# Performance work log

Measured on AMD Instinct MI355X. Metric: run time of the kernel, lower is better.

The kernel has to match this reference:

```python
import jax, jax.numpy as jnp
import numpy as np

B, S, D, H, E, K = 4, 2048, 1024, 4096, 8, 2
CAP = 2048      # expert capacity (tokens)
ALPHA = 0.01    # load-balance loss coefficient


def setup_inputs() -> dict:
    key = jax.random.key(0)
    ks = jax.random.split(key, 8)
    def w(k, shape, fan_in):
        return jax.random.normal(k, shape, jnp.float32) * (fan_in ** -0.5)
    return {
        "input": jax.random.normal(ks[0], (B, S, D), jnp.float32),
        "rw": w(ks[1], (D, E), D), "rb": jnp.zeros((E,), jnp.float32),
        "w1": w(ks[2], (E, D, H), D), "b1": jnp.zeros((E, H), jnp.float32),
        "w2": w(ks[3], (E, H, D), H), "b2": jnp.zeros((E, D), jnp.float32),
        "ow1": w(ks[4], (D, H), D), "ob1": jnp.zeros((H,), jnp.float32),
        "ow2": w(ks[5], (H, D), H), "ob2": jnp.zeros((D,), jnp.float32),
    }


def _moe(x, rw, rb, w1, b1, w2, b2, ow1, ob1, ow2, ob2):
    Bx, Sx, Dx = x.shape
    N = Bx * Sx
    xf = x.reshape(N, Dx)

    # --- router: softmax -> top-k -> renormalize ---
    scores = jax.nn.softmax(xf @ rw + rb, axis=-1)          # [N,E]
    tw, ti = jax.lax.top_k(scores, K)                       # [N,K]
    tw = tw / tw.sum(-1, keepdims=True)
    onehot = jax.nn.one_hot(ti, E, dtype=xf.dtype)          # [N,K,E]
    w_ne = jnp.einsum('nk,nke->ne', tw, onehot)             # combine weight per (token, expert)
    mask = onehot.sum(1) > 0                                # [N,E]
    mi = mask.astype(jnp.int32)

    # exclusive rank of each token within its expert's queue (token order, as torch nonzero())
    rank = jnp.cumsum(mi, axis=0) - mi                      # [N,E]
    within = mask & (rank < CAP)
    over = mask & (rank >= CAP)

    # --- dispatch within-capacity tokens into [E, CAP] slots (sentinel = N) ---
    tok = jnp.broadcast_to(jnp.arange(N, dtype=jnp.int32)[:, None], (N, E))
    eid = jnp.broadcast_to(jnp.arange(E, dtype=jnp.int32)[None, :], (N, E))
    slot = jnp.where(within, rank, CAP)                     # non-assigned -> pad column
    buf = jnp.full((E, CAP + 1), N, dtype=jnp.int32)
    buf = buf.at[eid.reshape(-1), slot.reshape(-1)].set(tok.reshape(-1))
    buf = buf[:, :CAP]                                      # [E,CAP]

    xpad = jnp.concatenate([xf, jnp.zeros((1, Dx), xf.dtype)], axis=0)
    xd = xpad[buf]                                          # [E,CAP,D]

    # --- grouped expert FFN (Linear -> relu -> Linear) ---
    h = jax.nn.relu(jnp.einsum('ecd,edh->ech', xd, w1) + b1[:, None, :])
    y = jnp.einsum('ech,ehd->ecd', h, w2) + b2[:, None, :]  # [E,CAP,D]

    # combine weights gathered per slot; pad slots get weight 0
    wpad = jnp.concatenate([w_ne, jnp.zeros((1, E), w_ne.dtype)], axis=0)
    wc = wpad[buf, jnp.arange(E, dtype=jnp.int32)[:, None]]  # [E,CAP]

    outpad = jnp.zeros((N + 1, Dx), xf.dtype)
    outpad = outpad.at[buf.reshape(-1)].add((wc[..., None] * y).reshape(-1, Dx))
    out = outpad[:N]

    # --- overflow tokens -> shared overflow FFN (computed densely, masked by weight) ---
    w_of = (w_ne * over.astype(w_ne.dtype)).sum(-1)          # [N]
    yo = jax.nn.relu(xf @ ow1 + ob1) @ ow2 + ob2             # [N,D]
    out = out + w_of[:, None] * yo

    # --- aux load-balance loss (detached in torch via .item()) ---
    num = mi.sum(0)                                          # [E]
    cnt = jnp.minimum(num, CAP)
    f = cnt.astype(xf.dtype) / N
    p = (w_ne * within.astype(w_ne.dtype)).sum(0) / jnp.maximum(cnt, 1).astype(xf.dtype)
    aux = ALPHA * E * jnp.sum(f * p)
    return out.reshape(Bx, Sx, Dx), jax.lax.stop_gradient(aux)


def reference(input, rw, rb, w1, b1, w2, b2, ow1, ob1, ow2, ob2):
    return _moe(input, rw, rb, w1, b1, w2, b2, ow1, ob1, ow2, ob2)
```

## Files before the change

### kernel.cpp

```cpp
#include <hip/hip_runtime.h>
#include <cstdint>

typedef __attribute__((ext_vector_type(8))) short bf16x8;
typedef __attribute__((ext_vector_type(4))) float f32x4;

#define N_TOK    8192
#define DMODEL   1024
#define HDIM     4096
#define CAPACITY 2048

__device__ __forceinline__ unsigned short f2bf(float f) {
  unsigned u = __float_as_uint(f);
  u += 0x7FFFu + ((u >> 16) & 1u);
  return (unsigned short)(u >> 16);
}

__device__ __forceinline__ void gl_lds16(const unsigned short* g, unsigned short* l) {
  __builtin_amdgcn_global_load_lds(
      (const __attribute__((address_space(1))) void*)g,
      (__attribute__((address_space(3))) void*)l, 16, 0, 0);
}

__global__ void cvtx_kernel(const float* __restrict__ x, unsigned short* __restrict__ xb) {
  long i0 = ((long)blockIdx.x * 256 + threadIdx.x) * 16;
#pragma unroll
  for (int ii = 0; ii < 4; ii++) {
    float4 v = *(const float4*)(x + i0 + ii * 4);
    ushort4 u;
    u.x = f2bf(v.x); u.y = f2bf(v.y); u.z = f2bf(v.z); u.w = f2bf(v.w);
    *(ushort4*)(xb + i0 + ii * 4) = u;
  }
}

__global__ void router_kernel(const float* __restrict__ x, const float* __restrict__ rw,
                              const float* __restrict__ rb, int4* __restrict__ recs) {
  int wave = threadIdx.x >> 6;
  int lane = threadIdx.x & 63;
  int tok = blockIdx.x * 4 + wave;
  const float* xr = x + (long)tok * DMODEL;
  float s[8];
#pragma unroll
  for (int e = 0; e < 8; e++) s[e] = 0.f;
  for (int ii = 0; ii < DMODEL / 64; ii++) {
    int k = lane + 64 * ii;
    float xv = xr[k];
    const float* wr = rw + k * 8;
    float4 a = *(const float4*)wr;
    float4 b = *(const float4*)(wr + 4);
    s[0] += xv * a.x; s[1] += xv * a.y; s[2] += xv * a.z; s[3] += xv * a.w;
    s[4] += xv * b.x; s[5] += xv * b.y; s[6] += xv * b.z; s[7] += xv * b.w;
  }
#pragma unroll
  for (int m = 1; m < 64; m <<= 1) {
#pragma unroll
    for (int e = 0; e < 8; e++) s[e] += __shfl_xor(s[e], m);
  }
  if (lane == 0) {
#pragma unroll
    for (int e = 0; e < 8; e++) s[e] += rb[e];
    int b0 = 0; float v0 = s[0];
#pragma unroll
    for (int e = 1; e < 8; e++) if (s[e] > v0) { v0 = s[e]; b0 = e; }
    int b1 = -1; float v1 = 0.f;
#pragma unroll
    for (int e = 0; e < 8; e++) {
      if (e == b0) continue;
      if (b1 < 0 || s[e] > v1) { v1 = s[e]; b1 = e; }
    }
    float t0 = 1.f / (1.f + expf(v1 - v0));
    float t1 = 1.f - t0;
    recs[tok] = make_int4(b0, b1, __float_as_int(t0), __float_as_int(t1));
  }
}

__device__ __forceinline__ int bump16(uint4& v, int e) {
  unsigned sh = (e & 1) ? 16u : 0u;
  unsigned inc = 1u << sh;
  unsigned old;
  switch (e >> 1) {
    case 0: old = v.x; v.x += inc; break;
    case 1: old = v.y; v.y += inc; break;
    case 2: old = v.z; v.z += inc; break;
    default: old = v.w; v.w += inc; break;
  }
  return (int)((old >> sh) & 0xFFFFu);
}

__device__ __forceinline__ unsigned field16(uint4 v, int e) {
  unsigned w;
  switch (e >> 1) { case 0: w = v.x; break; case 1: w = v.y; break; case 2: w = v.z; break; default: w = v.w; break; }
  return (w >> ((e & 1) ? 16 : 0)) & 0xFFFFu;
}

__global__ void assign_kernel(const int4* __restrict__ recs, int* __restrict__ buf,
                              float* __restrict__ wc, int* __restrict__ cnt,
                              float* __restrict__ auxOut) {
  __shared__ uint4 sc[1024];
  __shared__ unsigned sco[1024];
  __shared__ float pnum[8];
  int tid = threadIdx.x;
  if (tid < 8) pnum[tid] = 0.f;
  int4 rc[8];
#pragma unroll
  for (int i = 0; i < 8; i++) {
    rc[i] = recs[tid * 8 + i];
    rc[i].x &= 7; rc[i].y &= 7;
  }
  uint4 c; c.x = c.y = c.z = c.w = 0u;
#pragma unroll
  for (int i = 0; i < 8; i++) { bump16(c, rc[i].x); bump16(c, rc[i].y); }
  sc[tid] = c;
  __syncthreads();
  for (int off = 1; off < 1024; off <<= 1) {
    uint4 v; v.x = v.y = v.z = v.w = 0u;
    if (tid >= off) v = sc[tid - off];
    __syncthreads();
    sc[tid].x += v.x; sc[tid].y += v.y; sc[tid].z += v.z; sc[tid].w += v.w;
    __syncthreads();
  }
  uint4 base; base.x = base.y = base.z = base.w = 0u;
  if (tid > 0) base = sc[tid - 1];
  uint4 totals = sc[1023];

  uint4 run = base;
  float wof[8];
  unsigned oc = 0;
#pragma unroll
  for (int i = 0; i < 8; i++) {
    int tk = tid * 8 + i;
    int e0 = rc[i].x, e1 = rc[i].y;
    float w0 = __int_as_float(rc[i].z);
    float w1 = __int_as_float(rc[i].w);
    float w = 0.f;
    int r0 = bump16(run, e0);
    if (r0 < CAPACITY) {
      buf[e0 * CAPACITY + r0] = tk;
      wc[e0 * CAPACITY + r0] = w0;
      atomicAdd(&pnum[e0], w0);
    } else w += w0;
    int r1 = bump16(run, e1);
    if (r1 < CAPACITY) {
      buf[e1 * CAPACITY + r1] = tk;
      wc[e1 * CAPACITY + r1] = w1;
      atomicAdd(&pnum[e1], w1);
    } else w += w1;
    wof[i] = w;
    if (w > 0.f) oc++;
  }
  sco[tid] = oc;
  __syncthreads();
  for (int off = 1; off < 1024; off <<= 1) {
    unsigned v = (tid >= off) ? sco[tid - off] : 0u;
    __syncthreads();
    sco[tid] += v;
    __syncthreads();
  }
  unsigned ob = (tid > 0) ? sco[tid - 1] : 0u;
  unsigned Ot = sco[1023];
#pragma unroll
  for (int i = 0; i < 8; i++) {
    if (wof[i] > 0.f) {
      unsigned slot = ob++;
      int ve = 8 + (int)(slot >> 11);
      buf[ve * CAPACITY + (int)(slot & 2047)] = tid * 8 + i;
      wc[ve * CAPACITY + (int)(slot & 2047)] = wof[i];
    }
  }
  __syncthreads();
  if (tid == 0) {
    float aux = 0.f;
#pragma unroll
    for (int e = 0; e < 8; e++) {
      int tot = (int)field16(totals, e);
      int c2 = tot < CAPACITY ? tot : CAPACITY;
      cnt[e] = c2;
      float f = (float)c2 / (float)N_TOK;
      float p = pnum[e] / (float)(c2 > 1 ? c2 : 1);
      aux += f * p;
    }
#pragma unroll
    for (int i = 0; i < 4; i++) {
      int c2 = (int)Ot - i * CAPACITY;
      c2 = c2 < 0 ? 0 : (c2 > CAPACITY ? CAPACITY : c2);
      cnt[8 + i] = c2;
    }
    auxOut[0] = 0.01f * 8.f * aux;
  }
}

__global__ __launch_bounds__(256) void transpose_all(
    const float* __restrict__ w1, const float* __restrict__ w2,
    const float* __restrict__ ow1, const float* __restrict__ ow2,
    unsigned short* __restrict__ wt1, unsigned short* __restrict__ wt2,
    long slotStride, int pairBase) {
  int pair = pairBase + blockIdx.x / 2048;
  int t = blockIdx.x & 2047;
  long srcOff = (long)pair * DMODEL * HDIM;
  long dstOff = (long)(blockIdx.x / 2048) * slotStride;
  const float* in; unsigned short* out; int R, C;
  if (t < 1024) {
    in = (pair < 8) ? w1 + srcOff : ow1;
    out = wt1 + dstOff;
    R = DMODEL; C = HDIM;
  } else {
    in = (pair < 8) ? w2 + srcOff : ow2;
    out = wt2 + dstOff;
    R = HDIM; C = DMODEL;
    t -= 1024;
  }
  int tr = t / (C >> 6);
  int tc = t % (C >> 6);
  int r0 = tr << 6, c0 = tc << 6;
  __shared__ float tl[64][65];
  int row = threadIdx.x >> 4, cg = threadIdx.x & 15;
#pragma unroll
  for (int i = 0; i < 4; i++) {
    int r = row + 16 * i;
    float4 v = *(const float4*)(in + (long)(r0 + r) * C + c0 + cg * 4);
    tl[r][cg * 4 + 0] = v.x; tl[r][cg * 4 + 1] = v.y;
    tl[r][cg * 4 + 2] = v.z; tl[r][cg * 4 + 3] = v.w;
  }
  __syncthreads();
#pragma unroll
  for (int i = 0; i < 4; i++) {
    int oc = row + 16 * i;
    ushort4 o;
    o.x = f2bf(tl[cg * 4 + 0][oc]);
    o.y = f2bf(tl[cg * 4 + 1][oc]);
    o.z = f2bf(tl[cg * 4 + 2][oc]);
    o.w = f2bf(tl[cg * 4 + 3][oc]);
    *(ushort4*)(out + (long)(c0 + oc) * R + r0 + cg * 4) = o;
  }
}

__global__ __launch_bounds__(256) void gemm1_kernel(
    const unsigned short* __restrict__ xb, const int* __restrict__ buf,
    const int* __restrict__ cnt, const unsigned short* __restrict__ wt1, long wtStride,
    const float* __restrict__ b1, const float* __restrict__ ob1,
    unsigned short* __restrict__ h, long hStride, int eBase,
    const unsigned short* __restrict__ zp) {
  int q = gridDim.x >> 3;
  int bx = blockIdx.x;
  int id = (bx & 7) * q + (bx >> 3);
  int e = eBase + (id >> 9);
  int rem = id & 511;
  int mb = rem >> 5, nb = rem & 31;
  int m0 = mb * 128, n0 = nb * 128;
  if (m0 >= cnt[e]) return;
  const int* bufe = buf + e * CAPACITY;
  int slot = e < 8 ? e : 8;
  const unsigned short* wte = wt1 + (long)slot * wtStride;
  const float* bias = (e < 8) ? b1 + (long)e * HDIM : ob1;
  unsigned short* he = h + (long)e * hStride;

  __shared__ unsigned short As[128 * 64];
  __shared__ unsigned short Bs[128 * 64];

  int tid = threadIdx.x;
  int wave = tid >> 6, lane = tid & 63;
  int l15 = lane & 15, hi = lane >> 4;
  int mo = (wave >> 1) * 64, no = (wave & 1) * 64;

  int rlo = lane >> 3;
  int cg = (lane & 7) ^ rlo;
  const unsigned short* asrc[4];
  const unsigned short* bsrc[4];
#pragma unroll
  for (int j = 0; j < 4; j++) {
    int r = wave * 32 + j * 8 + rlo;
    int tok = bufe[m0 + r];
    asrc[j] = ((unsigned)tok < (unsigned)N_TOK) ? (xb + (long)tok * DMODEL + cg * 8)
                                                : (zp + cg * 8);
    bsrc[j] = wte + (long)(n0 + r) * DMODEL + cg * 8;
  }

  f32x4 zero4 = {0.f, 0.f, 0.f, 0.f};
  f32x4 acc[4][4];
#pragma unroll
  for (int mi = 0; mi < 4; mi++)
#pragma unroll
    for (int ni = 0; ni < 4; ni++) acc[mi][ni] = zero4;

  for (int k0 = 0; k0 < DMODEL; k0 += 64) {
#pragma unroll
    for (int j = 0; j < 4; j++) {
      gl_lds16(asrc[j] + k0, &As[wave * 2048 + j * 512]);
      gl_lds16(bsrc[j] + k0, &Bs[wave * 2048 + j * 512]);
    }
    __syncthreads();
#pragma unroll
    for (int ks = 0; ks < 2; ks++) {
      bf16x8 af[4], bfr[4];
#pragma unroll
      for (int mi = 0; mi < 4; mi++) {
        int r = mo + mi * 16 + l15;
        af[mi] = *(bf16x8*)&As[r * 64 + (((ks * 4 + hi) ^ (r & 7)) << 3)];
      }
#pragma unroll
      for (int ni = 0; ni < 4; ni++) {
        int r = no + ni * 16 + l15;
        bfr[ni] = *(bf16x8*)&Bs[r * 64 + (((ks * 4 + hi) ^ (r & 7)) << 3)];
      }
#pragma unroll
      for (int mi = 0; mi < 4; mi++)
#pragma unroll
        for (int ni = 0; ni < 4; ni++)
          acc[mi][ni] = __builtin_amdgcn_mfma_f32_16x16x32_bf16(af[mi], bfr[ni], acc[mi][ni], 0, 0, 0);
    }
    __syncthreads();
  }
#pragma unroll
  for (int ni = 0; ni < 4; ni++) {
    int col = n0 + no + ni * 16 + l15;
    float bv = bias[col];
#pragma unroll
    for (int mi = 0; mi < 4; mi++) {
#pragma unroll
      for (int j = 0; j < 4; j++) {
        int mr = m0 + mo + mi * 16 + hi * 4 + j;
        float val = acc[mi][ni][j] + bv;
        val = val > 0.f ? val : 0.f;
        he[(long)mr * HDIM + col] = f2bf(val);
      }
    }
  }
}

__global__ __launch_bounds__(256) void gemm2_kernel(
    const unsigned short* __restrict__ h, long hStride,
    const unsigned short* __restrict__ wt2, long wtStride,
    const float* __restrict__ b2, const float* __restrict__ ob2,
    const int* __restrict__ buf, const float* __restrict__ wc,
    const int* __restrict__ cnt, float* __restrict__ out,
    int eBase, int per, int klen) {
  int q = gridDim.x >> 3;
  int bx = blockIdx.x;
  int id = (bx & 7) * q + (bx >> 3);
  int e = eBase + id / per;
  int rem = id % per;
  int tile = rem & 127;
  int kc = rem >> 7;
  int mb = tile >> 3, nb = tile & 7;
  int m0 = mb * 128, n0 = nb * 128;
  if (m0 >= cnt[e]) return;
  const int* bufe = buf + e * CAPACITY;
  const float* wce = wc + e * CAPACITY;
  int slot = e < 8 ? e : 8;
  const unsigned short* wte = wt2 + (long)slot * wtStride;
  const float* bias = (e < 8) ? b2 + (long)e * DMODEL : ob2;
  const unsigned short* he = h + (long)e * hStride;
  int kbase = kc * klen;

  __shared__ unsigned short As[128 * 64];
  __shared__ unsigned short Bs[128 * 64];

  int tid = threadIdx.x;
  int wave = tid >> 6, lane = tid & 63;
  int l15 = lane & 15, hi = lane >> 4;
  int mo = (wave >> 1) * 64, no = (wave & 1) * 64;

  int rlo = lane >> 3;
  int cg = (lane & 7) ^ rlo;
  const unsigned short* asrc[4];
  const unsigned short* bsrc[4];
#pragma unroll
  for (int j = 0; j < 4; j++) {
    int r = wave * 32 + j * 8 + rlo;
    asrc[j] = he + (long)(m0 + r) * HDIM + cg * 8;
    bsrc[j] = wte + (long)(n0 + r) * HDIM + cg * 8;
  }

  f32x4 zero4 = {0.f, 0.f, 0.f, 0.f};
  f32x4 acc[4][4];
#pragma unroll
  for (int mi = 0; mi < 4; mi++)
#pragma unroll
    for (int ni = 0; ni < 4; ni++) acc[mi][ni] = zero4;

  for (int k0 = kbase; k0 < kbase + klen; k0 += 64) {
#pragma unroll
    for (int j = 0; j < 4; j++) {
      gl_lds16(asrc[j] + k0, &As[wave * 2048 + j * 512]);
      gl_lds16(bsrc[j] + k0, &Bs[wave * 2048 + j * 512]);
    }
    __syncthreads();
#pragma unroll
    for (int ks = 0; ks < 2; ks++) {
      bf16x8 af[4], bfr[4];
#pragma unroll
      for (int mi = 0; mi < 4; mi++) {
        int r = mo + mi * 16 + l15;
        af[mi] = *(bf16x8*)&As[r * 64 + (((ks * 4 + hi) ^ (r & 7)) << 3)];
      }
#pragma unroll
      for (int ni = 0; ni < 4; ni++) {
        int r = no + ni * 16 + l15;
        bfr[ni] = *(bf16x8*)&Bs[r * 64 + (((ks * 4 + hi) ^ (r & 7)) << 3)];
      }
#pragma unroll
      for (int mi = 0; mi < 4; mi++)
#pragma unroll
        for (int ni = 0; ni < 4; ni++)
          acc[mi][ni] = __builtin_amdgcn_mfma_f32_16x16x32_bf16(af[mi], bfr[ni], acc[mi][ni], 0, 0, 0);
    }
    __syncthreads();
  }
  float bcol[4];
#pragma unroll
  for (int ni = 0; ni < 4; ni++)
    bcol[ni] = (kc == 0) ? bias[n0 + no + ni * 16 + l15] : 0.f;
#pragma unroll
  for (int mi = 0; mi < 4; mi++) {
#pragma unroll
    for (int j = 0; j < 4; j++) {
      int m = m0 + mo + mi * 16 + hi * 4 + j;
      int t = bufe[m];
      if ((unsigned)t >= (unsigned)N_TOK) continue;
      float wv = wce[m];
      float* orow = out + (long)t * DMODEL;
#pragma unroll
      for (int ni = 0; ni < 4; ni++) {
        int col = n0 + no + ni * 16 + l15;
        float val = wv * (acc[mi][ni][j] + bcol[ni]);
        atomicAdd(orow + col, val);
      }
    }
  }
}

extern "C" void kernel_launch(void* const* d_in, const int* in_sizes, int n_in,
                              void* d_out, int out_size, void* d_ws, size_t ws_size,
                              hipStream_t stream) {
  const float* x   = (const float*)d_in[0];
  const float* rw  = (const float*)d_in[1];
  const float* rb  = (const float*)d_in[2];
  const float* w1  = (const float*)d_in[3];
  const float* b1  = (const float*)d_in[4];
  const float* w2  = (const float*)d_in[5];
  const float* b2  = (const float*)d_in[6];
  const float* ow1 = (const float*)d_in[7];
  const float* ob1 = (const float*)d_in[8];
  const float* ow2 = (const float*)d_in[9];
  const float* ob2 = (const float*)d_in[10];
  float* out = (float*)d_out;

  const long WSLOT = (long)DMODEL * HDIM;
  const long HSLOT = (long)CAPACITY * HDIM;

  bool fused = ws_size >= 380ull * 1024 * 1024;

  char* ws = (char*)d_ws;
  int4* recs = (int4*)(ws);
  int*  buf  = (int*)(ws + 131072);
  float* wcp = (float*)(ws + 229376);
  int*  cnt  = (int*)(ws + 327680);
  unsigned short* zp = (unsigned short*)(ws + 331776);
  unsigned short* xb  = (unsigned short*)(ws + 1048576);
  unsigned short* wt1 = (unsigned short*)(ws + 17825792);
  unsigned short* wt2;
  unsigned short* h;
  if (fused) {
    wt2 = (unsigned short*)(ws + 93323264);
    h   = (unsigned short*)(ws + 168820736);
  } else {
    wt2 = (unsigned short*)(ws + 26214400);
    h   = (unsigned short*)(ws + 34603008);
  }

  hipMemsetAsync(d_out, 0, (size_t)out_size * sizeof(float), stream);
  hipMemsetAsync(buf, 0xFF, 12 * CAPACITY * sizeof(int), stream);
  hipMemsetAsync(wcp, 0, 12 * CAPACITY * sizeof(float), stream);
  hipMemsetAsync(zp, 0, 2048, stream);

  cvtx_kernel<<<2048, 256, 0, stream>>>(x, xb);
  router_kernel<<<2048, 256, 0, stream>>>(x, rw, rb, recs);
  assign_kernel<<<1, 1024, 0, stream>>>(recs, buf, wcp, cnt, out + (long)N_TOK * DMODEL);

  if (fused) {
    transpose_all<<<9 * 2048, 256, 0, stream>>>(w1, w2, ow1, ow2, wt1, wt2, WSLOT, 0);
    gemm1_kernel<<<12 * 512, 256, 0, stream>>>(xb, buf, cnt, wt1, WSLOT, b1, ob1, h, HSLOT, 0, zp);
    gemm2_kernel<<<12 * 128, 256, 0, stream>>>(h, HSLOT, wt2, WSLOT, b2, ob2, buf, wcp, cnt, out,
                                               0, 128, HDIM);
  } else {
    for (int e = 0; e < 12; e++) {
      if (e <= 8)
        transpose_all<<<2048, 256, 0, stream>>>(w1, w2, ow1, ow2, wt1, wt2, 0, e);
      gemm1_kernel<<<512, 256, 0, stream>>>(xb, buf, cnt, wt1, 0, b1, ob1, h, 0, e, zp);
      gemm2_kernel<<<512, 256, 0, stream>>>(h, 0, wt2, 0, b2, ob2, buf, wcp, cnt, out,
                                            e, 512, HDIM / 4);
    }
  }
}
```

Baseline: 685.2 us.

## Use 256x256 tiles with 512-thread blocks and double-buffered LDS in expert GEMMs

Both expert GEMM kernels move from 128x128 tiles with 4 waves to 256x256 tiles with 8 waves, each wave owning a 128x64 sub-tile. The LDS staging is now double-buffered so the next K-slice loads while MFMAs run on the current one. The aim is more operand reuse per global byte and overlapping of loads with compute. GEMM2 split-K drops from 4 to 2 chunks, and the launch grids shrink to match. The costs are 128 KB of LDS per block and a much larger register footprint (128 accumulator floats plus fragments). Under launch_bounds(512,2) that footprint risks register spills and limits occupancy to one block per CU.

```diff
diff --git a/kernel.cpp b/kernel.cpp
--- a/kernel.cpp
+++ b/kernel.cpp
@@ -233,7 +233,16 @@
   }
 }
 
-__global__ __launch_bounds__(256) void gemm1_kernel(
+
+#define STAGE_PAIR(Abuf, Bbuf, kk)                                  \
+  do {                                                              \
+    _Pragma("unroll") for (int s = 0; s < 4; s++) {                 \
+      gl_lds16(asrc[s] + (kk), &(Abuf)[wave * 2048 + s * 512]);     \
+      gl_lds16(bsrc[s] + (kk), &(Bbuf)[wave * 2048 + s * 512]);     \
+    }                                                               \
+  } while (0)
+
+__global__ __launch_bounds__(512, 2) void gemm1_kernel(
     const unsigned short* __restrict__ xb, const int* __restrict__ buf,
     const int* __restrict__ cnt, const unsigned short* __restrict__ wt1, long wtStride,
     const float* __restrict__ b1, const float* __restrict__ ob1,
@@ -242,10 +251,10 @@
   int q = gridDim.x >> 3;
   int bx = blockIdx.x;
   int id = (bx & 7) * q + (bx >> 3);
-  int e = eBase + (id >> 9);
-  int rem = id & 511;
-  int mb = rem >> 5, nb = rem & 31;
-  int m0 = mb * 128, n0 = nb * 128;
+  int e = eBase + id / 128;
+  int rem = id % 128;
+  int mb = rem >> 4, nb = rem & 15;
+  int m0 = mb * 256, n0 = nb * 256;
   if (m0 >= cnt[e]) return;
   const int* bufe = buf + e * CAPACITY;
   int slot = e < 8 ? e : 8;
@@ -253,68 +262,74 @@
   const float* bias = (e < 8) ? b1 + (long)e * HDIM : ob1;
   unsigned short* he = h + (long)e * hStride;
 
-  __shared__ unsigned short As[128 * 64];
-  __shared__ unsigned short Bs[128 * 64];
+  __shared__ unsigned short As[2][256 * 64];
+  __shared__ unsigned short Bs[2][256 * 64];
 
   int tid = threadIdx.x;
   int wave = tid >> 6, lane = tid & 63;
   int l15 = lane & 15, hi = lane >> 4;
-  int mo = (wave >> 1) * 64, no = (wave & 1) * 64;
+  int wr = wave >> 2, wc = wave & 3;
+  int mo = wr * 128, no = wc * 64;
 
   int rlo = lane >> 3;
   int cg = (lane & 7) ^ rlo;
   const unsigned short* asrc[4];
   const unsigned short* bsrc[4];
 #pragma unroll
-  for (int j = 0; j < 4; j++) {
-    int r = wave * 32 + j * 8 + rlo;
+  for (int s = 0; s < 4; s++) {
+    int r = wave * 32 + s * 8 + rlo;
     int tok = bufe[m0 + r];
-    asrc[j] = ((unsigned)tok < (unsigned)N_TOK) ? (xb + (long)tok * DMODEL + cg * 8)
+    asrc[s] = ((unsigned)tok < (unsigned)N_TOK) ? (xb + (long)tok * DMODEL + cg * 8)
                                                 : (zp + cg * 8);
-    bsrc[j] = wte + (long)(n0 + r) * DMODEL + cg * 8;
+    bsrc[s] = wte + (long)(n0 + r) * DMODEL + cg * 8;
   }
 
   f32x4 zero4 = {0.f, 0.f, 0.f, 0.f};
-  f32x4 acc[4][4];
-#pragma unroll
-  for (int mi = 0; mi < 4; mi++)
+  f32x4 acc[8][4];
+#pragma unroll
+  for (int mi = 0; mi < 8; mi++)
 #pragma unroll
     for (int ni = 0; ni < 4; ni++) acc[mi][ni] = zero4;
 
-  for (int k0 = 0; k0 < DMODEL; k0 += 64) {
-#pragma unroll
-    for (int j = 0; j < 4; j++) {
-      gl_lds16(asrc[j] + k0, &As[wave * 2048 + j * 512]);
-      gl_lds16(bsrc[j] + k0, &Bs[wave * 2048 + j * 512]);
-    }
-    __syncthreads();
+  const int NT = DMODEL / 64;
+  STAGE_PAIR(As[0], Bs[0], 0);
+  __syncthreads();
+  int cur = 0;
+  for (int t = 0; t < NT; t++) {
+    if (t + 1 < NT) {
+      if (cur) STAGE_PAIR(As[0], Bs[0], (t + 1) * 64);
+      else     STAGE_PAIR(As[1], Bs[1], (t + 1) * 64);
+    }
+    const unsigned short* Ac = As[cur];
+    const unsigned short* Bc = Bs[cur];
 #pragma unroll
     for (int ks = 0; ks < 2; ks++) {
-      bf16x8 af[4], bfr[4];
-#pragma unroll
-      for (int mi = 0; mi < 4; mi++) {
+      bf16x8 af[8], bfv[4];
+#pragma unroll
+      for (int mi = 0; mi < 8; mi++) {
         int r = mo + mi * 16 + l15;
-        af[mi] = *(bf16x8*)&As[r * 64 + (((ks * 4 + hi) ^ (r & 7)) << 3)];
+        af[mi] = *(bf16x8*)&Ac[r * 64 + (((ks * 4 + hi) ^ (r & 7)) << 3)];
       }
 #pragma unroll
       for (int ni = 0; ni < 4; ni++) {
         int r = no + ni * 16 + l15;
-        bfr[ni] = *(bf16x8*)&Bs[r * 64 + (((ks * 4 + hi) ^ (r & 7)) << 3)];
+        bfv[ni] = *(bf16x8*)&Bc[r * 64 + (((ks * 4 + hi) ^ (r & 7)) << 3)];
       }
 #pragma unroll
-      for (int mi = 0; mi < 4; mi++)
+      for (int mi = 0; mi < 8; mi++)
 #pragma unroll
         for (int ni = 0; ni < 4; ni++)
-          acc[mi][ni] = __builtin_amdgcn_mfma_f32_16x16x32_bf16(af[mi], bfr[ni], acc[mi][ni], 0, 0, 0);
+          acc[mi][ni] = __builtin_amdgcn_mfma_f32_16x16x32_bf16(af[mi], bfv[ni], acc[mi][ni], 0, 0, 0);
     }
     __syncthreads();
+    cur ^= 1;
   }
 #pragma unroll
   for (int ni = 0; ni < 4; ni++) {
     int col = n0 + no + ni * 16 + l15;
     float bv = bias[col];
 #pragma unroll
-    for (int mi = 0; mi < 4; mi++) {
+    for (int mi = 0; mi < 8; mi++) {
 #pragma unroll
       for (int j = 0; j < 4; j++) {
         int mr = m0 + mo + mi * 16 + hi * 4 + j;
@@ -326,7 +341,7 @@
   }
 }
 
-__global__ __launch_bounds__(256) void gemm2_kernel(
+__global__ __launch_bounds__(512, 2) void gemm2_kernel(
     const unsigned short* __restrict__ h, long hStride,
     const unsigned short* __restrict__ wt2, long wtStride,
     const float* __restrict__ b2, const float* __restrict__ ob2,
@@ -338,10 +353,10 @@
   int id = (bx & 7) * q + (bx >> 3);
   int e = eBase + id / per;
   int rem = id % per;
-  int tile = rem & 127;
-  int kc = rem >> 7;
-  int mb = tile >> 3, nb = tile & 7;
-  int m0 = mb * 128, n0 = nb * 128;
+  int tile = rem & 31;
+  int kc = rem >> 5;
+  int mb = tile >> 2, nb = tile & 3;
+  int m0 = mb * 256, n0 = nb * 256;
   if (m0 >= cnt[e]) return;
   const int* bufe = buf + e * CAPACITY;
   const float* wce = wc + e * CAPACITY;
@@ -351,66 +366,72 @@
   const unsigned short* he = h + (long)e * hStride;
   int kbase = kc * klen;
 
-  __shared__ unsigned short As[128 * 64];
-  __shared__ unsigned short Bs[128 * 64];
+  __shared__ unsigned short As[2][256 * 64];
+  __shared__ unsigned short Bs[2][256 * 64];
 
   int tid = threadIdx.x;
   int wave = tid >> 6, lane = tid & 63;
   int l15 = lane & 15, hi = lane >> 4;
-  int mo = (wave >> 1) * 64, no = (wave & 1) * 64;
+  int wr = wave >> 2, wc2 = wave & 3;
+  int mo = wr * 128, no = wc2 * 64;
 
   int rlo = lane >> 3;
   int cg = (lane & 7) ^ rlo;
   const unsigned short* asrc[4];
   const unsigned short* bsrc[4];
 #pragma unroll
-  for (int j = 0; j < 4; j++) {
-    int r = wave * 32 + j * 8 + rlo;
-    asrc[j] = he + (long)(m0 + r) * HDIM + cg * 8;
-    bsrc[j] = wte + (long)(n0 + r) * HDIM + cg * 8;
+  for (int s = 0; s < 4; s++) {
+    int r = wave * 32 + s * 8 + rlo;
+    asrc[s] = he + (long)(m0 + r) * HDIM + kbase + cg * 8;
+    bsrc[s] = wte + (long)(n0 + r) * HDIM + kbase + cg * 8;
   }
 
   f32x4 zero4 = {0.f, 0.f, 0.f, 0.f};
-  f32x4 acc[4][4];
-#pragma unroll
-  for (int mi = 0; mi < 4; mi++)
+  f32x4 acc[8][4];
+#pragma unroll
+  for (int mi = 0; mi < 8; mi++)
 #pragma unroll
     for (int ni = 0; ni < 4; ni++) acc[mi][ni] = zero4;
 
-  for (int k0 = kbase; k0 < kbase + klen; k0 += 64) {
-#pragma unroll
-    for (int j = 0; j < 4; j++) {
-      gl_lds16(asrc[j] + k0, &As[wave * 2048 + j * 512]);
-      gl_lds16(bsrc[j] + k0, &Bs[wave * 2048 + j * 512]);
-    }
-    __syncthreads();
+  const int NT = klen / 64;
+  STAGE_PAIR(As[0], Bs[0], 0);
+  __syncthreads();
+  int cur = 0;
+  for (int t = 0; t < NT; t++) {
+    if (t + 1 < NT) {
+      if (cur) STAGE_PAIR(As[0], Bs[0], (t + 1) * 64);
+      else     STAGE_PAIR(As[1], Bs[1], (t + 1) * 64);
+    }
+    const unsigned short* Ac = As[cur];
+    const unsigned short* Bc = Bs[cur];
 #pragma unroll
     for (int ks = 0; ks < 2; ks++) {
-      bf16x8 af[4], bfr[4];
-#pragma unroll
-      for (int mi = 0; mi < 4; mi++) {
+      bf16x8 af[8], bfv[4];
+#pragma unroll
+      for (int mi = 0; mi < 8; mi++) {
         int r = mo + mi * 16 + l15;
-        af[mi] = *(bf16x8*)&As[r * 64 + (((ks * 4 + hi) ^ (r & 7)) << 3)];
+        af[mi] = *(bf16x8*)&Ac[r * 64 + (((ks * 4 + hi) ^ (r & 7)) << 3)];
       }
 #pragma unroll
       for (int ni = 0; ni < 4; ni++) {
         int r = no + ni * 16 + l15;
-        bfr[ni] = *(bf16x8*)&Bs[r * 64 + (((ks * 4 + hi) ^ (r & 7)) << 3)];
+        bfv[ni] = *(bf16x8*)&Bc[r * 64 + (((ks * 4 + hi) ^ (r & 7)) << 3)];
       }
 #pragma unroll
-      for (int mi = 0; mi < 4; mi++)
+      for (int mi = 0; mi < 8; mi++)
 #pragma unroll
         for (int ni = 0; ni < 4; ni++)
-          acc[mi][ni] = __builtin_amdgcn_mfma_f32_16x16x32_bf16(af[mi], bfr[ni], acc[mi][ni], 0, 0, 0);
+          acc[mi][ni] = __builtin_amdgcn_mfma_f32_16x16x32_bf16(af[mi], bfv[ni], acc[mi][ni], 0, 0, 0);
     }
     __syncthreads();
+    cur ^= 1;
   }
   float bcol[4];
 #pragma unroll
   for (int ni = 0; ni < 4; ni++)
     bcol[ni] = (kc == 0) ? bias[n0 + no + ni * 16 + l15] : 0.f;
 #pragma unroll
-  for (int mi = 0; mi < 4; mi++) {
+  for (int mi = 0; mi < 8; mi++) {
 #pragma unroll
     for (int j = 0; j < 4; j++) {
       int m = m0 + mo + mi * 16 + hi * 4 + j;
@@ -478,16 +499,16 @@
 
   if (fused) {
     transpose_all<<<9 * 2048, 256, 0, stream>>>(w1, w2, ow1, ow2, wt1, wt2, WSLOT, 0);
-    gemm1_kernel<<<12 * 512, 256, 0, stream>>>(xb, buf, cnt, wt1, WSLOT, b1, ob1, h, HSLOT, 0, zp);
-    gemm2_kernel<<<12 * 128, 256, 0, stream>>>(h, HSLOT, wt2, WSLOT, b2, ob2, buf, wcp, cnt, out,
-                                               0, 128, HDIM);
+    gemm1_kernel<<<12 * 128, 512, 0, stream>>>(xb, buf, cnt, wt1, WSLOT, b1, ob1, h, HSLOT, 0, zp);
+    gemm2_kernel<<<12 * 64, 512, 0, stream>>>(h, HSLOT, wt2, WSLOT, b2, ob2, buf, wcp, cnt, out,
+                                              0, 64, HDIM / 2);
   } else {
     for (int e = 0; e < 12; e++) {
       if (e <= 8)
         transpose_all<<<2048, 256, 0, stream>>>(w1, w2, ow1, ow2, wt1, wt2, 0, e);
-      gemm1_kernel<<<512, 256, 0, stream>>>(xb, buf, cnt, wt1, 0, b1, ob1, h, 0, e, zp);
-      gemm2_kernel<<<512, 256, 0, stream>>>(h, 0, wt2, 0, b2, ob2, buf, wcp, cnt, out,
-                                            e, 512, HDIM / 4);
-    }
-  }
-}
+      gemm1_kernel<<<128, 512, 0, stream>>>(xb, buf, cnt, wt1, 0, b1, ob1, h, 0, e, zp);
+      gemm2_kernel<<<64, 512, 0, stream>>>(h, 0, wt2, 0, b2, ob2, buf, wcp, cnt, out,
+                                           e, 64, HDIM / 2);
+    }
+  }
+}
```

Measured after the change: 654.1 us. 4.5% less time.
